# Kernel optimization log

Hardware: AMD Instinct MI355X
Metric: run time of the kernel (lower is better)

## Reference

```python
import jax, jax.numpy as jnp
import numpy as np

N_NODES = 20000
DIM = 512
N_EDGES = 320000
EPS = 1e-12  # torch F.normalize eps


def setup_inputs() -> dict:
    key = jax.random.key(0)
    k = jax.random.split(key, 6)
    scale = 1.0 / np.sqrt(DIM)
    return {
        "x": jax.random.normal(k[0], (N_NODES, DIM), dtype=jnp.float32),
        "edge_index": jax.random.randint(k[1], (2, N_EDGES), 0, N_NODES, dtype=jnp.int64),
        "W1": jax.random.normal(k[2], (DIM, DIM), dtype=jnp.float32) * scale,
        "b1": jnp.zeros((DIM,), dtype=jnp.float32),
        "W2": jax.random.normal(k[3], (DIM, DIM), dtype=jnp.float32) * scale,
        "b2": jnp.zeros((DIM,), dtype=jnp.float32),
        "alpha": jax.random.uniform(k[4], (), dtype=jnp.float32),
    }


def _gcn_conv(x, src, dst, norm, W, b, n):
    # x: [N, D]; src/dst: [E+N] (with self-loops); norm: [E+N]
    h = x @ W                              # [N, D] linear (no bias, like PyG lin)
    msg = h[src] * norm[:, None]           # gather + edgewise scale  [E+N, D]
    agg = jax.ops.segment_sum(msg, dst, num_segments=n)  # scatter-add [N, D]
    return agg + b


def _prep_edges(edge_index, n):
    loops = jnp.arange(n, dtype=edge_index.dtype)
    src = jnp.concatenate([edge_index[0], loops])
    dst = jnp.concatenate([edge_index[1], loops])
    deg = jax.ops.segment_sum(jnp.ones_like(dst, dtype=jnp.float32), dst, num_segments=n)
    dinv = jnp.where(deg > 0, jax.lax.rsqrt(deg), 0.0)
    norm = dinv[src] * dinv[dst]           # symmetric deg^{-1/2} normalization
    return src, dst, norm


def reference(x, edge_index, W1, b1, W2, b2, alpha):
    n = x.shape[0]
    src, dst, norm = _prep_edges(edge_index, n)
    h = _gcn_conv(x, src, dst, norm, W1, b1, n)
    h = jax.nn.relu(h)
    # dropout: eval mode -> identity
    h = _gcn_conv(h, src, dst, norm, W2, b2, n)
    a = jnp.clip(alpha, -1.0, 1.0)
    y = x + a * h
    nrm = jnp.maximum(jnp.linalg.norm(y, axis=-1, keepdims=True), EPS)
    return y / nrm
```

## Files before the change

### kernel.cpp

```cpp
#include <hip/hip_runtime.h>
#include <stdint.h>

#define DIMC 512
#define CAP 64

typedef __bf16 bf16_t;
typedef bf16_t bf16x8 __attribute__((ext_vector_type(8)));
typedef float f32x4 __attribute__((ext_vector_type(4)));
typedef float f32x2 __attribute__((ext_vector_type(2)));

__device__ __forceinline__ float4 ld4(const float* p) { return *(const float4*)p; }

typedef __attribute__((address_space(1))) void gvoid;
typedef __attribute__((address_space(3))) void svoid;

__device__ __forceinline__ void gload_lds16(const void* g, void* l) {
    __builtin_amdgcn_global_load_lds((gvoid*)(uintptr_t)g,
                                     (svoid*)(uint32_t)(uintptr_t)l, 16, 0, 0);
}

__device__ __forceinline__ uint8_t enc_fp8(float v) {
    return (uint8_t)(__builtin_amdgcn_cvt_pk_fp8_f32(v, v, 0, false) & 0xff);
}
__device__ __forceinline__ void dec8_fma(float* acc, uint2 u, float w) {
    f32x2 p0 = __builtin_amdgcn_cvt_pk_f32_fp8((int)u.x, false);
    f32x2 p1 = __builtin_amdgcn_cvt_pk_f32_fp8((int)u.x, true);
    f32x2 p2 = __builtin_amdgcn_cvt_pk_f32_fp8((int)u.y, false);
    f32x2 p3 = __builtin_amdgcn_cvt_pk_f32_fp8((int)u.y, true);
    acc[0] += p0.x * w; acc[1] += p0.y * w;
    acc[2] += p1.x * w; acc[3] += p1.y * w;
    acc[4] += p2.x * w; acc[5] += p2.y * w;
    acc[6] += p3.x * w; acc[7] += p3.y * w;
}

__global__ __launch_bounds__(256) void zero_kernel(int4* __restrict__ p, int n4) {
    int i = blockIdx.x * 256 + threadIdx.x;
    if (i < n4) p[i] = make_int4(0, 0, 0, 0);
}

__global__ __launch_bounds__(256) void prep_kernel(const float* __restrict__ x,
        bf16_t* __restrict__ xb, const float* __restrict__ W1,
        const float* __restrict__ W2, bf16_t* __restrict__ W1t,
        bf16_t* __restrict__ W2t, int n8, int nb_f2b,
        const int* __restrict__ ei, int E,
        int* __restrict__ cursor, int* __restrict__ csr) {
    __shared__ float tile[32][33];
    int b = blockIdx.x;
    if (b < nb_f2b) {
        int i = b * 256 + threadIdx.x;
        if (i >= n8) return;
        const float4* p = (const float4*)x + (size_t)i * 2;
        float4 a = p[0], c = p[1];
        bf16x8 o;
        o[0] = (bf16_t)a.x; o[1] = (bf16_t)a.y; o[2] = (bf16_t)a.z; o[3] = (bf16_t)a.w;
        o[4] = (bf16_t)c.x; o[5] = (bf16_t)c.y; o[6] = (bf16_t)c.z; o[7] = (bf16_t)c.w;
        ((bf16x8*)xb)[i] = o;
        return;
    }
    if (b < nb_f2b + 512) {
        int which = b - nb_f2b;
        const float* W = (which < 256) ? W1 : W2;
        bf16_t* Wt = (which < 256) ? W1t : W2t;
        int sub = which & 255;
        int bx = sub & 15, by = sub >> 4;
        int tx = threadIdx.x & 31, ty = threadIdx.x >> 5;
        for (int j = ty; j < 32; j += 8)
            tile[j][tx] = W[(size_t)(by * 32 + j) * DIMC + bx * 32 + tx];
        __syncthreads();
        for (int j = ty; j < 32; j += 8)
            Wt[(size_t)(bx * 32 + j) * DIMC + by * 32 + tx] = (bf16_t)tile[tx][j];
        return;
    }
    int e = (b - nb_f2b - 512) * 256 + threadIdx.x;
    if (e < E) {
        int s = ei[e], d = ei[E + e];
        int pos = atomicAdd(&cursor[d], 1);
        if (pos < CAP) csr[(size_t)d * CAP + pos] = s;
    }
}

template<bool FP8OUT>
__global__ __launch_bounds__(256) void gemm_mfma(const bf16_t* __restrict__ A,
        const bf16_t* __restrict__ Bt, void* __restrict__ Cout, int M) {
    __shared__ bf16_t As[2 * 4096];
    __shared__ bf16_t Bs[2 * 4096];
    const int t = threadIdx.x;
    const int lane = t & 63, wid = t >> 6;

    int nwg = gridDim.x * gridDim.y;
    int lin = blockIdx.y * gridDim.x + blockIdx.x;
    int q = nwg >> 3, r = nwg & 7;
    int k = lin & 7, i = lin >> 3;
    int mk = (k < r) ? k : r;
    int orig = k * q + mk + i;
    int bx2 = orig & 3, by2 = orig >> 2;
    const int m0 = by2 * 128, n0 = bx2 * 128;

    const bf16_t* asrc[2];
    const bf16_t* bsrc[2];
    char* aldst[2];
    char* bldst[2];
    #pragma unroll
    for (int q2 = 0; q2 < 2; ++q2) {
        int off = q2 * 4096 + wid * 1024 + lane * 16;
        int rr = off >> 6;
        int p = (off >> 4) & 3;
        int c = p ^ ((rr >> 1) & 3);
        int ga = m0 + rr; if (ga > M - 1) ga = M - 1;
        asrc[q2] = A + (size_t)ga * DIMC + c * 8;
        bsrc[q2] = Bt + (size_t)(n0 + rr) * DIMC + c * 8;
        aldst[q2] = (char*)As + q2 * 4096 + wid * 1024;
        bldst[q2] = (char*)Bs + q2 * 4096 + wid * 1024;
    }

    const int wr = wid >> 1, wc = wid & 1;
    int aoff[4], boff[4];
    #pragma unroll
    for (int i2 = 0; i2 < 4; ++i2) {
        int ra = wr * 64 + i2 * 16 + (lane & 15);
        int pa = (lane >> 4) ^ ((ra >> 1) & 3);
        aoff[i2] = ra * 64 + pa * 16;
        int rb = wc * 64 + i2 * 16 + (lane & 15);
        int pb = (lane >> 4) ^ ((rb >> 1) & 3);
        boff[i2] = rb * 64 + pb * 16;
    }

    #pragma unroll
    for (int q2 = 0; q2 < 2; ++q2) {
        gload_lds16(asrc[q2], aldst[q2]);
        gload_lds16(bsrc[q2], bldst[q2]);
    }

    f32x4 acc[4][4] = {};
    int cur = 0;
    for (int k0 = 0; k0 < DIMC; k0 += 32) {
        __syncthreads();
        if (k0 + 32 < DIMC) {
            int nxt = cur ^ 1;
            #pragma unroll
            for (int q2 = 0; q2 < 2; ++q2) {
                gload_lds16(asrc[q2] + k0 + 32, aldst[q2] + nxt * 8192);
                gload_lds16(bsrc[q2] + k0 + 32, bldst[q2] + nxt * 8192);
            }
        }
        const char* Ab = (const char*)As + cur * 8192;
        const char* Bb = (const char*)Bs + cur * 8192;
        bf16x8 av[4], bv[4];
        #pragma unroll
        for (int i2 = 0; i2 < 4; ++i2) av[i2] = *(const bf16x8*)(Ab + aoff[i2]);
        #pragma unroll
        for (int j = 0; j < 4; ++j) bv[j] = *(const bf16x8*)(Bb + boff[j]);
        #pragma unroll
        for (int i2 = 0; i2 < 4; ++i2)
            #pragma unroll
            for (int j = 0; j < 4; ++j)
                acc[i2][j] = __builtin_amdgcn_mfma_f32_16x16x32_bf16(av[i2], bv[j], acc[i2][j], 0, 0, 0);
        cur ^= 1;
    }

    #pragma unroll
    for (int i2 = 0; i2 < 4; ++i2) {
        int rbase = m0 + wr * 64 + i2 * 16 + (lane >> 4) * 4;
        #pragma unroll
        for (int rr = 0; rr < 4; ++rr) {
            int row = rbase + rr;
            if (row < M) {
                #pragma unroll
                for (int j = 0; j < 4; ++j) {
                    int col = n0 + wc * 64 + j * 16 + (lane & 15);
                    if (FP8OUT)
                        ((uint8_t*)Cout)[(size_t)row * DIMC + col] = enc_fp8(acc[i2][j][rr]);
                    else
                        ((bf16_t*)Cout)[(size_t)row * DIMC + col] = (bf16_t)acc[i2][j][rr];
                }
            }
        }
    }
}

__global__ __launch_bounds__(256) void agg_relu_kernel(const uint8_t* __restrict__ H8,
        const int* __restrict__ csr, const int* __restrict__ cursor,
        const float* __restrict__ bias, bf16_t* __restrict__ G, int n) {
    int node = (blockIdx.x * blockDim.x + threadIdx.x) >> 6;
    if (node >= n) return;
    int lane = threadIdx.x & 63;
    int c0 = lane * 8;
    int deg = cursor[node];
    float dv = rsqrtf((float)(deg + 1));
    int dl = (deg < CAP) ? deg : CAP;
    const uint8_t* Hc = H8 + c0;
    float acc[8] = {};
    dec8_fma(acc, *(const uint2*)(Hc + (size_t)node * DIMC), dv);
    const int* crow = csr + (size_t)node * CAP;
    int e = 0;
    for (; e + 8 <= dl; e += 8) {
        int idx[8]; float wt[8]; uint2 r[8];
        #pragma unroll
        for (int j = 0; j < 8; ++j) idx[j] = crow[e + j];
        #pragma unroll
        for (int j = 0; j < 8; ++j) wt[j] = rsqrtf((float)(cursor[idx[j]] + 1));
        #pragma unroll
        for (int j = 0; j < 8; ++j) r[j] = *(const uint2*)(Hc + (size_t)idx[j] * DIMC);
        #pragma unroll
        for (int j = 0; j < 8; ++j) dec8_fma(acc, r[j], wt[j]);
    }
    for (; e < dl; ++e) {
        int s0 = crow[e];
        float w0 = rsqrtf((float)(cursor[s0] + 1));
        dec8_fma(acc, *(const uint2*)(Hc + (size_t)s0 * DIMC), w0);
    }
    float4 b0 = ld4(bias + c0), b1 = ld4(bias + c0 + 4);
    float bb[8] = {b0.x, b0.y, b0.z, b0.w, b1.x, b1.y, b1.z, b1.w};
    bf16x8 o;
    #pragma unroll
    for (int j = 0; j < 8; ++j) o[j] = (bf16_t)fmaxf(dv * acc[j] + bb[j], 0.f);
    *(bf16x8*)(G + (size_t)node * DIMC + c0) = o;
}

__global__ __launch_bounds__(256) void agg_final_kernel(const uint8_t* __restrict__ H8,
        const bf16_t* __restrict__ xb, const int* __restrict__ csr,
        const int* __restrict__ cursor, const float* __restrict__ bias,
        const float* __restrict__ alphaPtr, float* __restrict__ out, int n) {
    int node = (blockIdx.x * blockDim.x + threadIdx.x) >> 6;
    if (node >= n) return;
    int lane = threadIdx.x & 63;
    int c0 = lane * 8;
    int deg = cursor[node];
    float dv = rsqrtf((float)(deg + 1));
    int dl = (deg < CAP) ? deg : CAP;
    const uint8_t* Hc = H8 + c0;
    float acc[8] = {};
    dec8_fma(acc, *(const uint2*)(Hc + (size_t)node * DIMC), dv);
    const int* crow = csr + (size_t)node * CAP;
    int e = 0;
    for (; e + 8 <= dl; e += 8) {
        int idx[8]; float wt[8]; uint2 r[8];
        #pragma unroll
        for (int j = 0; j < 8; ++j) idx[j] = crow[e + j];
        #pragma unroll
        for (int j = 0; j < 8; ++j) wt[j] = rsqrtf((float)(cursor[idx[j]] + 1));
        #pragma unroll
        for (int j = 0; j < 8; ++j) r[j] = *(const uint2*)(Hc + (size_t)idx[j] * DIMC);
        #pragma unroll
        for (int j = 0; j < 8; ++j) dec8_fma(acc, r[j], wt[j]);
    }
    for (; e < dl; ++e) {
        int s0 = crow[e];
        float w0 = rsqrtf((float)(cursor[s0] + 1));
        dec8_fma(acc, *(const uint2*)(Hc + (size_t)s0 * DIMC), w0);
    }
    float al = alphaPtr[0];
    al = fminf(fmaxf(al, -1.f), 1.f);
    float4 b0 = ld4(bias + c0), b1 = ld4(bias + c0 + 4);
    float bb[8] = {b0.x, b0.y, b0.z, b0.w, b1.x, b1.y, b1.z, b1.w};
    bf16x8 xv = *(const bf16x8*)(xb + (size_t)node * DIMC + c0);
    float y[8];
    float ss = 0.f;
    #pragma unroll
    for (int j = 0; j < 8; ++j) {
        y[j] = (float)xv[j] + al * (dv * acc[j] + bb[j]);
        ss += y[j] * y[j];
    }
    #pragma unroll
    for (int off = 1; off < 64; off <<= 1) ss += __shfl_xor(ss, off);
    float sc = 1.f / fmaxf(sqrtf(ss), 1e-12f);
    float* op = out + (size_t)node * DIMC + c0;
    *(float4*)op = make_float4(y[0] * sc, y[1] * sc, y[2] * sc, y[3] * sc);
    *(float4*)(op + 4) = make_float4(y[4] * sc, y[5] * sc, y[6] * sc, y[7] * sc);
}

extern "C" void kernel_launch(void* const* d_in, const int* in_sizes, int n_in,
                              void* d_out, int out_size, void* d_ws, size_t ws_size,
                              hipStream_t stream) {
    const float* x     = (const float*)d_in[0];
    const int*   ei    = (const int*)d_in[1];
    const float* W1    = (const float*)d_in[2];
    const float* b1    = (const float*)d_in[3];
    const float* W2    = (const float*)d_in[4];
    const float* b2    = (const float*)d_in[5];
    const float* alpha = (const float*)d_in[6];
    float* out = (float*)d_out;

    const int N = in_sizes[0] / DIMC;
    const int E = in_sizes[1] / 2;
    const size_t MN = (size_t)N * DIMC;

    char* w = (char*)d_ws;
    auto carve = [&](size_t bytes) {
        void* p = (void*)w;
        w += (bytes + 255) & ~(size_t)255;
        return p;
    };
    uint8_t* H8a   = (uint8_t*)carve(MN);
    uint8_t* H8b   = (uint8_t*)carve(MN);
    bf16_t* Gb     = (bf16_t*)carve(MN * sizeof(bf16_t));
    bf16_t* xb     = (bf16_t*)carve(MN * sizeof(bf16_t));
    bf16_t* W1t    = (bf16_t*)carve((size_t)DIMC * DIMC * sizeof(bf16_t));
    bf16_t* W2t    = (bf16_t*)carve((size_t)DIMC * DIMC * sizeof(bf16_t));
    int*    cursor = (int*)carve(((size_t)N + 4) * sizeof(int));
    int*    csr    = (int*)carve((size_t)N * CAP * sizeof(int));

    int blocks_e = (E + 255) / 256;
    int n4 = (N + 3) / 4;
    zero_kernel<<<(n4 + 255) / 256, 256, 0, stream>>>((int4*)cursor, n4);

    int n8 = (int)(MN / 8);
    int nb_f2b = (n8 + 255) / 256;
    prep_kernel<<<nb_f2b + 512 + blocks_e, 256, 0, stream>>>(
        x, xb, W1, W2, W1t, W2t, n8, nb_f2b, ei, E, cursor, csr);

    dim3 gg(DIMC / 128, (N + 127) / 128);
    int aggBlocks = (N + 3) / 4;
    gemm_mfma<true><<<gg, 256, 0, stream>>>(xb, W1t, (void*)H8a, N);
    agg_relu_kernel<<<aggBlocks, 256, 0, stream>>>(H8a, csr, cursor, b1, Gb, N);
    gemm_mfma<true><<<gg, 256, 0, stream>>>(Gb, W2t, (void*)H8b, N);
    agg_final_kernel<<<aggBlocks, 256, 0, stream>>>(H8b, xb, csr, cursor, b2, alpha, out, N);
}
```

Baseline: 134.7 us.

## Double GEMM K-tile to 64 and coarsen prep kernel work per block

The GEMM now stages 64-wide K slices per iteration with a wider XOR swizzle, which halves the number of barriers and main-loop iterations and doubles LDS use to 64 KB per block. The prep kernel now gives each thread 8 conversion items and 4 edge items, and each transpose block handles both weight matrices, so far fewer blocks are launched. The larger LDS footprint may lower GEMM occupancy.

After: 125.0 us. 7.2% less time.

```diff
diff --git a/kernel.cpp b/kernel.cpp
--- a/kernel.cpp
+++ b/kernel.cpp
@@ -47,43 +47,55 @@
     __shared__ float tile[32][33];
     int b = blockIdx.x;
     if (b < nb_f2b) {
-        int i = b * 256 + threadIdx.x;
-        if (i >= n8) return;
-        const float4* p = (const float4*)x + (size_t)i * 2;
-        float4 a = p[0], c = p[1];
-        bf16x8 o;
-        o[0] = (bf16_t)a.x; o[1] = (bf16_t)a.y; o[2] = (bf16_t)a.z; o[3] = (bf16_t)a.w;
-        o[4] = (bf16_t)c.x; o[5] = (bf16_t)c.y; o[6] = (bf16_t)c.z; o[7] = (bf16_t)c.w;
-        ((bf16x8*)xb)[i] = o;
+        int base = b * 2048 + threadIdx.x;
+        #pragma unroll
+        for (int it = 0; it < 8; ++it) {
+            int i = base + it * 256;
+            if (i < n8) {
+                const float4* p = (const float4*)x + (size_t)i * 2;
+                float4 a = p[0], c = p[1];
+                bf16x8 o;
+                o[0] = (bf16_t)a.x; o[1] = (bf16_t)a.y; o[2] = (bf16_t)a.z; o[3] = (bf16_t)a.w;
+                o[4] = (bf16_t)c.x; o[5] = (bf16_t)c.y; o[6] = (bf16_t)c.z; o[7] = (bf16_t)c.w;
+                ((bf16x8*)xb)[i] = o;
+            }
+        }
         return;
     }
-    if (b < nb_f2b + 512) {
-        int which = b - nb_f2b;
-        const float* W = (which < 256) ? W1 : W2;
-        bf16_t* Wt = (which < 256) ? W1t : W2t;
-        int sub = which & 255;
+    if (b < nb_f2b + 256) {
+        int sub = b - nb_f2b;
         int bx = sub & 15, by = sub >> 4;
         int tx = threadIdx.x & 31, ty = threadIdx.x >> 5;
-        for (int j = ty; j < 32; j += 8)
-            tile[j][tx] = W[(size_t)(by * 32 + j) * DIMC + bx * 32 + tx];
-        __syncthreads();
-        for (int j = ty; j < 32; j += 8)
-            Wt[(size_t)(bx * 32 + j) * DIMC + by * 32 + tx] = (bf16_t)tile[tx][j];
+        #pragma unroll
+        for (int which = 0; which < 2; ++which) {
+            const float* W = which ? W2 : W1;
+            bf16_t* Wt = which ? W2t : W1t;
+            if (which) __syncthreads();
+            for (int j = ty; j < 32; j += 8)
+                tile[j][tx] = W[(size_t)(by * 32 + j) * DIMC + bx * 32 + tx];
+            __syncthreads();
+            for (int j = ty; j < 32; j += 8)
+                Wt[(size_t)(bx * 32 + j) * DIMC + by * 32 + tx] = (bf16_t)tile[tx][j];
+        }
         return;
     }
-    int e = (b - nb_f2b - 512) * 256 + threadIdx.x;
-    if (e < E) {
-        int s = ei[e], d = ei[E + e];
-        int pos = atomicAdd(&cursor[d], 1);
-        if (pos < CAP) csr[(size_t)d * CAP + pos] = s;
+    int base = (b - nb_f2b - 256) * 1024 + threadIdx.x;
+    #pragma unroll
+    for (int it = 0; it < 4; ++it) {
+        int e = base + it * 256;
+        if (e < E) {
+            int s = ei[e], d = ei[E + e];
+            int pos = atomicAdd(&cursor[d], 1);
+            if (pos < CAP) csr[(size_t)d * CAP + pos] = s;
+        }
     }
 }
 
 template<bool FP8OUT>
 __global__ __launch_bounds__(256) void gemm_mfma(const bf16_t* __restrict__ A,
         const bf16_t* __restrict__ Bt, void* __restrict__ Cout, int M) {
-    __shared__ bf16_t As[2 * 4096];
-    __shared__ bf16_t Bs[2 * 4096];
+    __shared__ bf16_t As[2 * 8192];
+    __shared__ bf16_t Bs[2 * 8192];
     const int t = threadIdx.x;
     const int lane = t & 63, wid = t >> 6;
 
@@ -96,65 +108,68 @@
     int bx2 = orig & 3, by2 = orig >> 2;
     const int m0 = by2 * 128, n0 = bx2 * 128;
 
-    const bf16_t* asrc[2];
-    const bf16_t* bsrc[2];
-    char* aldst[2];
-    char* bldst[2];
-    #pragma unroll
-    for (int q2 = 0; q2 < 2; ++q2) {
+    const bf16_t* asrc[4];
+    const bf16_t* bsrc[4];
+    int ldoff[4];
+    #pragma unroll
+    for (int q2 = 0; q2 < 4; ++q2) {
         int off = q2 * 4096 + wid * 1024 + lane * 16;
-        int rr = off >> 6;
-        int p = (off >> 4) & 3;
-        int c = p ^ ((rr >> 1) & 3);
+        int rr = off >> 7;
+        int p = (off >> 4) & 7;
+        int c = p ^ (rr & 7);
         int ga = m0 + rr; if (ga > M - 1) ga = M - 1;
         asrc[q2] = A + (size_t)ga * DIMC + c * 8;
         bsrc[q2] = Bt + (size_t)(n0 + rr) * DIMC + c * 8;
-        aldst[q2] = (char*)As + q2 * 4096 + wid * 1024;
-        bldst[q2] = (char*)Bs + q2 * 4096 + wid * 1024;
+        ldoff[q2] = q2 * 4096 + wid * 1024;
     }
 
     const int wr = wid >> 1, wc = wid & 1;
-    int aoff[4], boff[4];
+    int aoff[4][2], boff[4][2];
     #pragma unroll
     for (int i2 = 0; i2 < 4; ++i2) {
         int ra = wr * 64 + i2 * 16 + (lane & 15);
-        int pa = (lane >> 4) ^ ((ra >> 1) & 3);
-        aoff[i2] = ra * 64 + pa * 16;
         int rb = wc * 64 + i2 * 16 + (lane & 15);
-        int pb = (lane >> 4) ^ ((rb >> 1) & 3);
-        boff[i2] = rb * 64 + pb * 16;
-    }
-
-    #pragma unroll
-    for (int q2 = 0; q2 < 2; ++q2) {
-        gload_lds16(asrc[q2], aldst[q2]);
-        gload_lds16(bsrc[q2], bldst[q2]);
+        #pragma unroll
+        for (int ks = 0; ks < 2; ++ks) {
+            int ca = ks * 4 + (lane >> 4);
+            aoff[i2][ks] = ra * 128 + (ca ^ (ra & 7)) * 16;
+            boff[i2][ks] = rb * 128 + (ca ^ (rb & 7)) * 16;
+        }
+    }
+
+    #pragma unroll
+    for (int q2 = 0; q2 < 4; ++q2) {
+        gload_lds16(asrc[q2], (char*)As + ldoff[q2]);
+        gload_lds16(bsrc[q2], (char*)Bs + ldoff[q2]);
     }
 
     f32x4 acc[4][4] = {};
     int cur = 0;
-    for (int k0 = 0; k0 < DIMC; k0 += 32) {
+    for (int k0 = 0; k0 < DIMC; k0 += 64) {
         __syncthreads();
-        if (k0 + 32 < DIMC) {
+        if (k0 + 64 < DIMC) {
             int nxt = cur ^ 1;
             #pragma unroll
-            for (int q2 = 0; q2 < 2; ++q2) {
-                gload_lds16(asrc[q2] + k0 + 32, aldst[q2] + nxt * 8192);
-                gload_lds16(bsrc[q2] + k0 + 32, bldst[q2] + nxt * 8192);
+            for (int q2 = 0; q2 < 4; ++q2) {
+                gload_lds16(asrc[q2] + k0 + 64, (char*)As + nxt * 16384 + ldoff[q2]);
+                gload_lds16(bsrc[q2] + k0 + 64, (char*)Bs + nxt * 16384 + ldoff[q2]);
             }
         }
-        const char* Ab = (const char*)As + cur * 8192;
-        const char* Bb = (const char*)Bs + cur * 8192;
-        bf16x8 av[4], bv[4];
-        #pragma unroll
-        for (int i2 = 0; i2 < 4; ++i2) av[i2] = *(const bf16x8*)(Ab + aoff[i2]);
-        #pragma unroll
-        for (int j = 0; j < 4; ++j) bv[j] = *(const bf16x8*)(Bb + boff[j]);
-        #pragma unroll
-        for (int i2 = 0; i2 < 4; ++i2)
+        const char* Ab = (const char*)As + cur * 16384;
+        const char* Bb = (const char*)Bs + cur * 16384;
+        #pragma unroll
+        for (int ks = 0; ks < 2; ++ks) {
+            bf16x8 av[4], bv[4];
             #pragma unroll
-            for (int j = 0; j < 4; ++j)
-                acc[i2][j] = __builtin_amdgcn_mfma_f32_16x16x32_bf16(av[i2], bv[j], acc[i2][j], 0, 0, 0);
+            for (int i2 = 0; i2 < 4; ++i2) av[i2] = *(const bf16x8*)(Ab + aoff[i2][ks]);
+            #pragma unroll
+            for (int j = 0; j < 4; ++j) bv[j] = *(const bf16x8*)(Bb + boff[j][ks]);
+            #pragma unroll
+            for (int i2 = 0; i2 < 4; ++i2)
+                #pragma unroll
+                for (int j = 0; j < 4; ++j)
+                    acc[i2][j] = __builtin_amdgcn_mfma_f32_16x16x32_bf16(av[i2], bv[j], acc[i2][j], 0, 0, 0);
+        }
         cur ^= 1;
     }
 
@@ -300,13 +315,13 @@
     int*    cursor = (int*)carve(((size_t)N + 4) * sizeof(int));
     int*    csr    = (int*)carve((size_t)N * CAP * sizeof(int));
 
-    int blocks_e = (E + 255) / 256;
     int n4 = (N + 3) / 4;
     zero_kernel<<<(n4 + 255) / 256, 256, 0, stream>>>((int4*)cursor, n4);
 
     int n8 = (int)(MN / 8);
-    int nb_f2b = (n8 + 255) / 256;
-    prep_kernel<<<nb_f2b + 512 + blocks_e, 256, 0, stream>>>(
+    int nb_f2b = (n8 + 2047) / 2048;
+    int nb_fill = (E + 1023) / 1024;
+    prep_kernel<<<nb_f2b + 256 + nb_fill, 256, 0, stream>>>(
         x, xb, W1, W2, W1t, W2t, n8, nb_f2b, ei, E, cursor, csr);
 
     dim3 gg(DIMC / 128, (N + 127) / 128);
```
